# Optimization experiments

Hardware: AMD Instinct MI355X
Metric: run time of the kernel (lower is better)

The kernel has to match this reference:

```python
import jax, jax.numpy as jnp
import numpy as np

N, NF, D, H, L, FFN, E, EF = 2048, 64, 256, 8, 6, 1024, 32768, 16
HD = D // H
MAXDEG, MAXDIST = 64, 8


def setup_inputs() -> dict:
    key = jax.random.key(0)
    ks = jax.random.split(key, 32)
    s = 0.02
    nrm = lambda k, sh: (jax.random.normal(k, sh, jnp.float32) * s)
    return {
        "x": jax.random.normal(ks[0], (N, NF), jnp.float32),
        "edge_attr": jax.random.normal(ks[1], (E, EF), jnp.float32),
        "node_proj_w": nrm(ks[2], (D, NF)),
        "node_proj_b": jnp.zeros((D,), jnp.float32),
        "in_deg_emb": nrm(ks[3], (MAXDEG + 1, D)),
        "out_deg_emb": nrm(ks[4], (MAXDEG + 1, D)),
        "dist_bias": nrm(ks[5], (MAXDIST + 2, H)),
        "edge_proj_w": nrm(ks[6], (H, EF)),
        "edge_proj_b": jnp.zeros((H,), jnp.float32),
        "cls_token": nrm(ks[7], (1, D)),
        "q_w": nrm(ks[8], (L, D, D)), "q_b": jnp.zeros((L, D)),
        "k_w": nrm(ks[9], (L, D, D)), "k_b": jnp.zeros((L, D)),
        "v_w": nrm(ks[10], (L, D, D)), "v_b": jnp.zeros((L, D)),
        "o_w": nrm(ks[11], (L, D, D)), "o_b": jnp.zeros((L, D)),
        "ffn1_w": nrm(ks[12], (L, FFN, D)), "ffn1_b": jnp.zeros((L, FFN)),
        "ffn2_w": nrm(ks[13], (L, D, FFN)), "ffn2_b": jnp.zeros((L, D)),
        "ln1_s": jnp.ones((L, D)), "ln1_b": jnp.zeros((L, D)),
        "ln2_s": jnp.ones((L, D)), "ln2_b": jnp.zeros((L, D)),
        "fn_s": jnp.ones((D,)), "fn_b": jnp.zeros((D,)),
        "edge_index": jax.random.randint(ks[14], (2, E), 0, N, dtype=jnp.int32),
        "dist_matrix": jax.random.randint(ks[15], (N, N), 0, MAXDIST + 2, dtype=jnp.int32),
    }


def _ln(v, s, b):
    m = v.mean(-1, keepdims=True)
    va = v.var(-1, keepdims=True)
    return (v - m) / jnp.sqrt(va + 1e-5) * s + b


def _forward(x, edge_attr, node_proj_w, node_proj_b, in_deg_emb, out_deg_emb,
             dist_bias, edge_proj_w, edge_proj_b, cls_token,
             q_w, q_b, k_w, k_b, v_w, v_b, o_w, o_b,
             ffn1_w, ffn1_b, ffn2_w, ffn2_b,
             ln1_s, ln1_b, ln2_s, ln2_b, fn_s, fn_b,
             edge_index, dist_matrix):
    # node embedding + degree encoding
    h = x @ node_proj_w.T + node_proj_b  # (N, D)
    ones = jnp.ones((E,), jnp.int32)
    in_deg = jnp.clip(jax.ops.segment_sum(ones, edge_index[1], num_segments=N), 0, MAXDEG)
    out_deg = jnp.clip(jax.ops.segment_sum(ones, edge_index[0], num_segments=N), 0, MAXDEG)
    h = h + in_deg_emb[in_deg] + out_deg_emb[out_deg]
    h = jnp.concatenate([cls_token, h], axis=0)  # (N+1, D), CLS at row 0
    Nf = N + 1
    # spatial bias: pad dist matrix with zeros for CLS, then embed
    dist_p = jnp.pad(jnp.clip(dist_matrix, 0, MAXDIST + 1), ((1, 0), (1, 0)))
    bias = dist_bias[dist_p]  # (Nf, Nf, H)
    # edge-feature bias: scatter-add projected edge features into dense (N,N,H)
    proj = edge_attr @ edge_proj_w.T + edge_proj_b  # (E, H)
    ebias = jnp.zeros((N, N, H), h.dtype).at[edge_index[0], edge_index[1]].add(proj)
    bias = bias + jnp.pad(ebias, ((1, 0), (1, 0), (0, 0)))
    bias_t = bias.transpose(2, 0, 1)  # (H, Nf, Nf)
    scale = np.sqrt(HD).astype(np.float32)
    for l in range(L):
        hn = _ln(h, ln1_s[l], ln1_b[l])
        Q = (hn @ q_w[l].T + q_b[l]).reshape(Nf, H, HD).transpose(1, 0, 2)
        K = (hn @ k_w[l].T + k_b[l]).reshape(Nf, H, HD).transpose(1, 0, 2)
        V = (hn @ v_w[l].T + v_b[l]).reshape(Nf, H, HD).transpose(1, 0, 2)
        logits = jnp.einsum('hnd,hmd->hnm', Q, K) / scale + bias_t
        attn = jax.nn.softmax(logits, axis=-1)
        o = jnp.einsum('hnm,hmd->hnd', attn, V).transpose(1, 0, 2).reshape(Nf, D)
        h = h + o @ o_w[l].T + o_b[l]
        hn2 = _ln(h, ln2_s[l], ln2_b[l])
        h = h + jax.nn.gelu(hn2 @ ffn1_w[l].T + ffn1_b[l], approximate=False) @ ffn2_w[l].T + ffn2_b[l]
    h = _ln(h, fn_s, fn_b)
    return h, h[0]


def reference(x, edge_attr, node_proj_w, node_proj_b, in_deg_emb, out_deg_emb,
              dist_bias, edge_proj_w, edge_proj_b, cls_token,
              q_w, q_b, k_w, k_b, v_w, v_b, o_w, o_b,
              ffn1_w, ffn1_b, ffn2_w, ffn2_b,
              ln1_s, ln1_b, ln2_s, ln2_b, fn_s, fn_b,
              edge_index, dist_matrix):
    return _forward(x, edge_attr, node_proj_w, node_proj_b, in_deg_emb, out_deg_emb,
                    dist_bias, edge_proj_w, edge_proj_b, cls_token,
                    q_w, q_b, k_w, k_b, v_w, v_b, o_w, o_b,
                    ffn1_w, ffn1_b, ffn2_w, ffn2_b,
                    ln1_s, ln1_b, ln2_s, ln2_b, fn_s, fn_b,
                    edge_index, dist_matrix)
```

## Files before the change

kernel.cpp:

```cpp
#include <hip/hip_runtime.h>
#include <math.h>

#define N_ 2048
#define NF_IN 64
#define D_ 256
#define H_ 8
#define HD_ 32
#define L_ 6
#define FFN_ 1024
#define E_ 32768
#define EF_ 16
#define NF 2049
#define MAXDEG_ 64
#define BSTRIDE 2112
#define RPAD 2112
#define NSPLIT 4

typedef __attribute__((ext_vector_type(8))) short bf16x8;
typedef __attribute__((ext_vector_type(4))) float f32x4;

__device__ inline unsigned short f2b(float f){
  union { float f; unsigned u; } v; v.f = f;
  unsigned r = (v.u + 0x7fffu + ((v.u >> 16) & 1u)) >> 16;
  return (unsigned short)r;
}

__device__ inline unsigned char f2fp8(float f){
  unsigned u = __float_as_uint(f);
  unsigned s = (u >> 24) & 0x80u;
  float a = fabsf(f);
  if (a >= 448.f) return (unsigned char)(s | 0x7Eu);
  if (a < 0.015625f){
    int k = (int)rintf(a * 512.f);
    return (unsigned char)(s | (unsigned)k);
  }
  int e; float m = frexpf(a, &e);
  int E = e - 1;
  int m3 = (int)rintf(m * 16.f) - 8;
  if (m3 == 8){ E++; m3 = 0; }
  if (E > 8){ E = 8; m3 = 6; }
  if (E == 8 && m3 > 6) m3 = 6;
  return (unsigned char)(s | (unsigned)((E + 7) << 3) | (unsigned)m3);
}
__device__ inline float fp82f(unsigned char b){
  return __builtin_amdgcn_cvt_f32_fp8((int)b, 0);
}

__device__ inline void atomic_add_fp8(unsigned char* p, float add){
  unsigned* wp = (unsigned*)((size_t)p & ~(size_t)3);
  int sh = (int)((size_t)p & 3) * 8;
  unsigned old = *wp, assumed;
  do {
    assumed = old;
    unsigned char cur = (unsigned char)((assumed >> sh) & 0xFFu);
    float f = fp82f(cur) + add;
    unsigned nw = (assumed & ~(0xFFu << sh)) | ((unsigned)f2fp8(f) << sh);
    old = atomicCAS(wp, assumed, nw);
  } while (old != assumed);
}

__device__ inline float wred_sum(float v){
  #pragma unroll
  for (int o = 32; o > 0; o >>= 1) v += __shfl_down(v, o, 64);
  return v;
}

__global__ void zero_int(int* p, int n){
  int i = blockIdx.x * blockDim.x + threadIdx.x;
  if (i < n) p[i] = 0;
}

__global__ void deg_count(const int* __restrict__ ei, int* __restrict__ ind,
                          int* __restrict__ outd){
  int e = blockIdx.x * blockDim.x + threadIdx.x;
  if (e >= E_) return;
  atomicAdd(&outd[ei[e]], 1);
  atomicAdd(&ind[ei[E_ + e]], 1);
}

__global__ void embed_k(const float* __restrict__ x, const float* __restrict__ W,
                        const float* __restrict__ b, const float* __restrict__ inE,
                        const float* __restrict__ outE, const int* __restrict__ ind,
                        const int* __restrict__ outd, const float* __restrict__ cls,
                        float* __restrict__ h){
  int i = blockIdx.x, d = threadIdx.x;
  if (i == 0){ h[d] = cls[d]; return; }
  int n = i - 1;
  const float4* xr = (const float4*)(x + (long)n * NF_IN);
  const float4* wr = (const float4*)(W + (long)d * NF_IN);
  float acc = b[d];
  #pragma unroll
  for (int k = 0; k < NF_IN / 4; k++){
    float4 a = xr[k], w = wr[k];
    acc += a.x * w.x + a.y * w.y + a.z * w.z + a.w * w.w;
  }
  int id = min(ind[n], MAXDEG_), od = min(outd[n], MAXDEG_);
  acc += inE[(long)id * D_ + d] + outE[(long)od * D_ + d];
  h[(long)i * D_ + d] = acc;
}

__global__ void bias_fill(const int* __restrict__ dist, const float* __restrict__ db,
                          unsigned char* __restrict__ bb){
  __shared__ unsigned char lut8[10][H_];
  int i = blockIdx.x;
  if (threadIdx.x < 80) ((unsigned char*)lut8)[threadIdx.x] = f2fp8(db[threadIdx.x]);
  __syncthreads();
  for (int u = threadIdx.x; u < BSTRIDE / 8; u += 256){
    int dp[8];
    #pragma unroll
    for (int k = 0; k < 8; k++){
      int j = u * 8 + k;
      int d = 0;
      if (i > 0 && j > 0 && j < NF){
        int dv = dist[(long)(i - 1) * N_ + (j - 1)];
        d = max(0, min(dv, 9));
      }
      dp[k] = (j < NF) ? d : -1;
    }
    #pragma unroll
    for (int h = 0; h < H_; h++){
      unsigned lo = 0, hi = 0;
      #pragma unroll
      for (int k = 0; k < 4; k++){
        unsigned b0 = (dp[k] >= 0) ? lut8[dp[k]][h] : 0u;
        unsigned b1 = (dp[4 + k] >= 0) ? lut8[dp[4 + k]][h] : 0u;
        lo |= b0 << (8 * k);
        hi |= b1 << (8 * k);
      }
      *(uint2*)(bb + ((long)h * NF + i) * BSTRIDE + u * 8) = make_uint2(lo, hi);
    }
  }
}

__global__ void edge_bias(const float* __restrict__ ea, const float* __restrict__ W,
                          const float* __restrict__ b, const int* __restrict__ ei,
                          unsigned char* __restrict__ bb){
  int e = blockIdx.x * blockDim.x + threadIdx.x;
  if (e >= E_) return;
  float a[EF_];
  #pragma unroll
  for (int k = 0; k < EF_; k++) a[k] = ea[(long)e * EF_ + k];
  int src = ei[e], dst = ei[E_ + e];
  #pragma unroll
  for (int h = 0; h < H_; h++){
    float p = b[h];
    #pragma unroll
    for (int k = 0; k < EF_; k++) p += a[k] * W[h * EF_ + k];
    atomic_add_fp8(bb + ((long)h * NF + src + 1) * BSTRIDE + (dst + 1), p);
  }
}

__global__ void w2b_all(const float* __restrict__ qw, const float* __restrict__ kw,
                        const float* __restrict__ vw, const float* __restrict__ ow,
                        const float* __restrict__ f1w, const float* __restrict__ f2w,
                        short* __restrict__ wqkv, short* __restrict__ owb,
                        short* __restrict__ f1wb, short* __restrict__ f2wb){
  long i = (long)blockIdx.x * 256 + threadIdx.x;
  const long DD = (long)D_ * D_, LDD = (long)L_ * DD, LFD = (long)L_ * FFN_ * D_;
  if (i < LDD){
    long l = i / DD, r = i - l * DD;
    wqkv[l * 3 * DD + r]          = (short)f2b(qw[i]);
    wqkv[l * 3 * DD + DD + r]     = (short)f2b(kw[i]);
    wqkv[l * 3 * DD + 2 * DD + r] = (short)f2b(vw[i]);
    owb[i] = (short)f2b(ow[i]);
  }
  if (i < LFD){
    f1wb[i] = (short)f2b(f1w[i]);
    f2wb[i] = (short)f2b(f2w[i]);
  }
}

__global__ void ln_k(const float* __restrict__ in, const float* __restrict__ s,
                     const float* __restrict__ b, float* __restrict__ outf,
                     short* __restrict__ outb, int dup0){
  __shared__ float r1[4], r2[4];
  int i = blockIdx.x, d = threadIdx.x;
  float v = in[(long)i * D_ + d];
  float s1 = wred_sum(v), s2 = wred_sum(v * v);
  if ((d & 63) == 0){ r1[d >> 6] = s1; r2[d >> 6] = s2; }
  __syncthreads();
  float S1 = r1[0] + r1[1] + r1[2] + r1[3];
  float S2 = r2[0] + r2[1] + r2[2] + r2[3];
  float m = S1 * (1.0f / D_);
  float var = S2 * (1.0f / D_) - m * m;
  float y = (v - m) * rsqrtf(var + 1e-5f) * s[d] + b[d];
  if (outf){
    outf[(long)i * D_ + d] = y;
    if (dup0 && i == 0) outf[(long)NF * D_ + d] = y;
  }
  if (outb) outb[(long)i * D_ + d] = (short)f2b(y);
}

__global__ __launch_bounds__(256) void qkv_gemm(const short* __restrict__ A,
    const short* __restrict__ Wall, const float* __restrict__ qb,
    const float* __restrict__ kb, const float* __restrict__ vb,
    short* __restrict__ QKb, short* __restrict__ Vtg, int l){
  const int z = blockIdx.z;
  const short* W = Wall + ((long)(l * 3 + z)) * D_ * D_;
  const float* bsp = (z == 0) ? qb : (z == 1) ? kb : vb;
  __shared__ __align__(16) short As[64][40], Ws[64][40];
  const int tid = threadIdx.x, lane = tid & 63, wave = tid >> 6;
  const int col = lane & 15, quad = lane >> 4;
  const int wm = wave & 1, wn = wave >> 1;
  const int bm = blockIdx.x * 64, bn = blockIdx.y * 64;
  const f32x4 zero4 = {0.f, 0.f, 0.f, 0.f};
  f32x4 acc[2][2] = {{zero4, zero4}, {zero4, zero4}};
  const int row = tid >> 2, seg = tid & 3;
  for (int k0 = 0; k0 < D_; k0 += 32){
    __syncthreads();
    bf16x8 av = (bf16x8)(short)0;
    int gm = bm + row;
    if (gm < NF) av = *(const bf16x8*)(A + (long)gm * D_ + k0 + seg * 8);
    *(bf16x8*)&As[row][seg * 8] = av;
    *(bf16x8*)&Ws[row][seg * 8] = *(const bf16x8*)(W + (long)(bn + row) * D_ + k0 + seg * 8);
    __syncthreads();
    bf16x8 a0 = *(const bf16x8*)&As[wm * 32 + col][quad * 8];
    bf16x8 a1 = *(const bf16x8*)&As[wm * 32 + 16 + col][quad * 8];
    bf16x8 b0 = *(const bf16x8*)&Ws[wn * 32 + col][quad * 8];
    bf16x8 b1 = *(const bf16x8*)&Ws[wn * 32 + 16 + col][quad * 8];
    acc[0][0] = __builtin_amdgcn_mfma_f32_16x16x32_bf16(a0, b0, acc[0][0], 0, 0, 0);
    acc[0][1] = __builtin_amdgcn_mfma_f32_16x16x32_bf16(a0, b1, acc[0][1], 0, 0, 0);
    acc[1][0] = __builtin_amdgcn_mfma_f32_16x16x32_bf16(a1, b0, acc[1][0], 0, 0, 0);
    acc[1][1] = __builtin_amdgcn_mfma_f32_16x16x32_bf16(a1, b1, acc[1][1], 0, 0, 0);
  }
  #pragma unroll
  for (int i = 0; i < 2; i++)
    #pragma unroll
    for (int j = 0; j < 2; j++)
      #pragma unroll
      for (int r = 0; r < 4; r++){
        int gm = bm + wm * 32 + i * 16 + quad * 4 + r;
        if (gm >= NF) continue;
        int gn = bn + wn * 32 + j * 16 + col;
        float v = acc[i][j][r] + bsp[gn];
        if (z < 2) QKb[(long)z * NF * D_ + (long)gm * D_ + gn] = (short)f2b(v);
        else       Vtg[(long)gn * BSTRIDE + gm] = (short)f2b(v);
      }
}

template<int ACT, int ATOM, int MERGE>
__global__ __launch_bounds__(256) void mgemm(const short* __restrict__ A,
    const float* __restrict__ Op, const float* __restrict__ Lp,
    const short* __restrict__ W, const float* __restrict__ bs,
    float* __restrict__ Cf, short* __restrict__ Cb,
    int M, int Nn, int Kc, int Kstride){
  __shared__ __align__(16) short As[64][40], Ws[64][40];
  const int tid = threadIdx.x, lane = tid & 63, wave = tid >> 6;
  const int col = lane & 15, quad = lane >> 4;
  const int wm = wave & 1, wn = wave >> 1;
  const int bm = blockIdx.x * 64, bn = blockIdx.y * 64;
  const int koff = blockIdx.z * Kc;
  const f32x4 zero4 = {0.f, 0.f, 0.f, 0.f};
  f32x4 acc[2][2] = {{zero4, zero4}, {zero4, zero4}};
  const int row = tid >> 2, seg = tid & 3;
  for (int k0 = 0; k0 < Kc; k0 += 32){
    __syncthreads();
    int gm = bm + row;
    if (MERGE){
      int kg = koff + k0 + seg * 8;
      int hh = kg >> 5, d0 = kg & 31;
      short sarr[8] = {0,0,0,0,0,0,0,0};
      if (gm < M){
        float o0=0,o1=0,o2=0,o3=0,o4=0,o5=0,o6=0,o7=0, sl=0.f;
        #pragma unroll
        for (int q = 0; q < NSPLIT; q++){
          long rb = (long)(q * H_ + hh) * RPAD + gm;
          const float* op = Op + rb * HD_ + d0;
          float4 v0 = *(const float4*)op, v1 = *(const float4*)(op + 4);
          o0 += v0.x; o1 += v0.y; o2 += v0.z; o3 += v0.w;
          o4 += v1.x; o5 += v1.y; o6 += v1.z; o7 += v1.w;
          sl += Lp[rb];
        }
        float inv = 1.0f / sl;
        sarr[0]=(short)f2b(o0*inv); sarr[1]=(short)f2b(o1*inv);
        sarr[2]=(short)f2b(o2*inv); sarr[3]=(short)f2b(o3*inv);
        sarr[4]=(short)f2b(o4*inv); sarr[5]=(short)f2b(o5*inv);
        sarr[6]=(short)f2b(o6*inv); sarr[7]=(short)f2b(o7*inv);
      }
      *(bf16x8*)&As[row][seg * 8] = *(bf16x8*)sarr;
    } else {
      bf16x8 av = (bf16x8)(short)0;
      if (gm < M) av = *(const bf16x8*)(A + (long)gm * Kstride + koff + k0 + seg * 8);
      *(bf16x8*)&As[row][seg * 8] = av;
    }
    *(bf16x8*)&Ws[row][seg * 8] =
      *(const bf16x8*)(W + (long)(bn + row) * Kstride + koff + k0 + seg * 8);
    __syncthreads();
    bf16x8 a0 = *(const bf16x8*)&As[wm * 32 + col][quad * 8];
    bf16x8 a1 = *(const bf16x8*)&As[wm * 32 + 16 + col][quad * 8];
    bf16x8 b0 = *(const bf16x8*)&Ws[wn * 32 + col][quad * 8];
    bf16x8 b1 = *(const bf16x8*)&Ws[wn * 32 + 16 + col][quad * 8];
    acc[0][0] = __builtin_amdgcn_mfma_f32_16x16x32_bf16(a0, b0, acc[0][0], 0, 0, 0);
    acc[0][1] = __builtin_amdgcn_mfma_f32_16x16x32_bf16(a0, b1, acc[0][1], 0, 0, 0);
    acc[1][0] = __builtin_amdgcn_mfma_f32_16x16x32_bf16(a1, b0, acc[1][0], 0, 0, 0);
    acc[1][1] = __builtin_amdgcn_mfma_f32_16x16x32_bf16(a1, b1, acc[1][1], 0, 0, 0);
  }
  #pragma unroll
  for (int i = 0; i < 2; i++)
    #pragma unroll
    for (int j = 0; j < 2; j++)
      #pragma unroll
      for (int r = 0; r < 4; r++){
        int gm = bm + wm * 32 + i * 16 + quad * 4 + r;
        if (gm >= M) continue;
        int gn = bn + wn * 32 + j * 16 + col;
        if (ATOM){
          float v = acc[i][j][r] + (blockIdx.z == 0 ? bs[gn] : 0.f);
          atomicAdd(&Cf[(long)gm * Nn + gn], v);
        } else {
          float v = acc[i][j][r] + bs[gn];
          if (ACT == 1) v = v * 0.5f * (1.0f + erff(v * 0.70710678118654752f));
          Cb[(long)gm * Nn + gn] = (short)f2b(v);
        }
      }
}

__global__ __launch_bounds__(256) void fattn_k(const short* __restrict__ Qb,
    const short* __restrict__ Kb, const short* __restrict__ Vtg,
    const unsigned char* __restrict__ bias8, float* __restrict__ Opart,
    float* __restrict__ Lpart){
  __shared__ __align__(16) short Ks[64][40];
  __shared__ __align__(16) short Vt[32][72];
  __shared__ __align__(16) unsigned char PS[4][2304];

  const int tid = threadIdx.x, wave = tid >> 6, lane = tid & 63;
  const int col = lane & 15, quad = lane >> 4;
  const int h = blockIdx.y, qz = blockIdx.z;
  const int i0 = blockIdx.x * 64 + wave * 16;
  const int t0 = (qz == 0) ? 0 : 9 + 8 * (qz - 1);
  const int t1 = t0 + ((qz == 0) ? 9 : 8);

  int qrow = min(i0 + col, NF - 1);
  bf16x8 qf = *(const bf16x8*)(Qb + (long)qrow * D_ + h * HD_ + quad * 8);

  f32x4 oacc0 = {0.f, 0.f, 0.f, 0.f}, oacc1 = {0.f, 0.f, 0.f, 0.f};
  float rs[4] = {0.f, 0.f, 0.f, 0.f};
  const f32x4 zero4 = {0.f, 0.f, 0.f, 0.f};
  const float scale = 0.17677669529663687f;
  short* Pp = (short*)PS[wave];

  for (int t = t0; t < t1; t++){
    const int j0 = t * 64;
    __syncthreads();
    {
      int key = tid >> 2, seg = tid & 3;
      int j = j0 + key;
      bf16x8 kv = (bf16x8)(short)0;
      if (j < NF) kv = *(const bf16x8*)(Kb + (long)j * D_ + h * HD_ + seg * 8);
      *(bf16x8*)&Ks[key][seg * 8] = kv;
    }
    {
      int d = tid >> 3, seg = tid & 7;
      *(bf16x8*)&Vt[d][seg * 8] =
        *(const bf16x8*)(Vtg + (long)(h * HD_ + d) * BSTRIDE + j0 + seg * 8);
    }
    {
      int rw = lane >> 2, seg = lane & 3;
      int irow = min(i0 + rw, NF - 1);
      uint4 bv = *(const uint4*)(bias8 + (long)(h * NF + irow) * BSTRIDE + j0 + seg * 16);
      uint2* d2 = (uint2*)&PS[wave][rw * 80 + seg * 16];
      d2[0] = make_uint2(bv.x, bv.y);
      d2[1] = make_uint2(bv.z, bv.w);
    }
    __syncthreads();

    f32x4 sacc[4];
    #pragma unroll
    for (int t4 = 0; t4 < 4; t4++){
      bf16x8 kf = *(const bf16x8*)&Ks[t4 * 16 + col][quad * 8];
      sacc[t4] = __builtin_amdgcn_mfma_f32_16x16x32_bf16(qf, kf, zero4, 0, 0, 0);
    }

    const bool tail = (j0 + 64 > NF);
    #pragma unroll
    for (int r = 0; r < 4; r++){
      #pragma unroll
      for (int t4 = 0; t4 < 4; t4++){
        float bv = fp82f(PS[wave][(quad * 4 + r) * 80 + t4 * 16 + col]);
        float p = __expf(sacc[t4][r] * scale + bv);
        if (tail && (j0 + t4 * 16 + col >= NF)) p = 0.f;
        rs[r] += p;
        sacc[t4][r] = p;
      }
    }
    #pragma unroll
    for (int r = 0; r < 4; r++)
      #pragma unroll
      for (int t4 = 0; t4 < 4; t4++)
        Pp[(quad * 4 + r) * 72 + t4 * 16 + col] = (short)f2b(sacc[t4][r]);

    #pragma unroll
    for (int ks = 0; ks < 2; ks++){
      bf16x8 af = *(const bf16x8*)&Pp[col * 72 + ks * 32 + quad * 8];
      bf16x8 v0 = *(const bf16x8*)&Vt[col][ks * 32 + quad * 8];
      bf16x8 v1 = *(const bf16x8*)&Vt[16 + col][ks * 32 + quad * 8];
      oacc0 = __builtin_amdgcn_mfma_f32_16x16x32_bf16(af, v0, oacc0, 0, 0, 0);
      oacc1 = __builtin_amdgcn_mfma_f32_16x16x32_bf16(af, v1, oacc1, 0, 0, 0);
    }
  }

  #pragma unroll
  for (int r = 0; r < 4; r++){
    #pragma unroll
    for (int o = 1; o < 16; o <<= 1) rs[r] += __shfl_xor(rs[r], o, 64);
  }
  long pi = ((long)qz * H_ + h) * RPAD + i0 + quad * 4;
  #pragma unroll
  for (int r = 0; r < 4; r++){
    Opart[(pi + r) * HD_ + col] = oacc0[r];
    Opart[(pi + r) * HD_ + 16 + col] = oacc1[r];
    if (col == 0) Lpart[pi + r] = rs[r];
  }
}

extern "C" void kernel_launch(void* const* d_in, const int* in_sizes, int n_in,
                              void* d_out, int out_size, void* d_ws, size_t ws_size,
                              hipStream_t stream){
  const float* x    = (const float*)d_in[0];
  const float* ea   = (const float*)d_in[1];
  const float* npw  = (const float*)d_in[2];
  const float* npb  = (const float*)d_in[3];
  const float* inE  = (const float*)d_in[4];
  const float* outE = (const float*)d_in[5];
  const float* db   = (const float*)d_in[6];
  const float* epw  = (const float*)d_in[7];
  const float* epb  = (const float*)d_in[8];
  const float* cls  = (const float*)d_in[9];
  const float* qw   = (const float*)d_in[10];
  const float* qb   = (const float*)d_in[11];
  const float* kw   = (const float*)d_in[12];
  const float* kb   = (const float*)d_in[13];
  const float* vw   = (const float*)d_in[14];
  const float* vb   = (const float*)d_in[15];
  const float* ow   = (const float*)d_in[16];
  const float* ob   = (const float*)d_in[17];
  const float* f1w  = (const float*)d_in[18];
  const float* f1b  = (const float*)d_in[19];
  const float* f2w  = (const float*)d_in[20];
  const float* f2bp = (const float*)d_in[21];
  const float* ln1s = (const float*)d_in[22];
  const float* ln1b = (const float*)d_in[23];
  const float* ln2s = (const float*)d_in[24];
  const float* ln2b = (const float*)d_in[25];
  const float* fns  = (const float*)d_in[26];
  const float* fnb  = (const float*)d_in[27];
  const int*   ei   = (const int*)d_in[28];
  const int*   dist = (const int*)d_in[29];

  float* ws = (float*)d_ws;
  long off = 0;
  float* h     = ws + off; off += (long)NF * D_;
  float* Opart = ws + off; off += (long)NSPLIT * H_ * RPAD * HD_;
  float* Lpart = ws + off; off += (long)NSPLIT * H_ * RPAD;
  unsigned char* bias8 = (unsigned char*)(ws + off);
  off += ((long)H_ * NF * BSTRIDE + 3) / 4;
  short* hnb   = (short*)(ws + off); off += ((long)NF * D_ + 1) / 2;
  short* QKb   = (short*)(ws + off); off += (long)NF * D_;
  short* Vtg   = (short*)(ws + off); off += ((long)D_ * BSTRIDE + 1) / 2;
  short* midb  = (short*)(ws + off); off += ((long)NF * FFN_ + 1) / 2;
  short* wqkv  = (short*)(ws + off); off += ((long)3 * L_ * D_ * D_ + 1) / 2;
  short* owb   = (short*)(ws + off); off += ((long)L_ * D_ * D_ + 1) / 2;
  short* f1wb  = (short*)(ws + off); off += ((long)L_ * FFN_ * D_ + 1) / 2;
  short* f2wb  = (short*)(ws + off); off += ((long)L_ * FFN_ * D_ + 1) / 2;
  int*   ind   = (int*)(ws + off);
  int*   outd  = ind + N_;

  zero_int<<<(2 * N_ + 255) / 256, 256, 0, stream>>>(ind, 2 * N_);
  deg_count<<<(E_ + 255) / 256, 256, 0, stream>>>(ei, ind, outd);
  embed_k<<<NF, D_, 0, stream>>>(x, npw, npb, inE, outE, ind, outd, cls, h);
  bias_fill<<<NF, 256, 0, stream>>>(dist, db, bias8);
  edge_bias<<<(E_ + 255) / 256, 256, 0, stream>>>(ea, epw, epb, ei, bias8);
  {
    long LFD = (long)L_ * FFN_ * D_;
    w2b_all<<<(int)((LFD + 255) / 256), 256, 0, stream>>>(qw, kw, vw, ow, f1w, f2w,
                                                          wqkv, owb, f1wb, f2wb);
  }

  dim3 gQKV((NF + 63) / 64, D_ / 64, 3);
  dim3 gO((NF + 63) / 64, D_ / 64, 2);
  dim3 gF((NF + 63) / 64, FFN_ / 64, 1);
  dim3 gF2((NF + 63) / 64, D_ / 64, 4);
  dim3 gA((NF + 63) / 64, H_, NSPLIT);
  for (int l = 0; l < L_; l++){
    ln_k<<<NF, D_, 0, stream>>>(h, ln1s + l * D_, ln1b + l * D_, nullptr, hnb, 0);
    qkv_gemm<<<gQKV, 256, 0, stream>>>(hnb, wqkv, qb + l * D_, kb + l * D_, vb + l * D_,
                                       QKb, Vtg, l);
    fattn_k<<<gA, 256, 0, stream>>>(QKb, QKb + (long)NF * D_, Vtg, bias8, Opart, Lpart);
    mgemm<0,1,1><<<gO, 256, 0, stream>>>(nullptr, Opart, Lpart,
                                         owb + (long)l * D_ * D_, ob + l * D_,
                                         h, nullptr, NF, D_, 128, D_);
    ln_k<<<NF, D_, 0, stream>>>(h, ln2s + l * D_, ln2b + l * D_, nullptr, hnb, 0);
    mgemm<1,0,0><<<gF, 256, 0, stream>>>(hnb, nullptr, nullptr,
                                         f1wb + (long)l * FFN_ * D_, f1b + l * FFN_,
                                         nullptr, midb, NF, FFN_, D_, D_);
    mgemm<0,1,0><<<gF2, 256, 0, stream>>>(midb, nullptr, nullptr,
                                          f2wb + (long)l * FFN_ * D_, f2bp + l * D_,
                                          h, nullptr, NF, D_, 256, FFN_);
  }
  ln_k<<<NF, D_, 0, stream>>>(h, fns, fnb, (float*)d_out, nullptr, 1);
}
```

Baseline: 686.1 us.

## Fold softmax scale into Q and log2e into bias, load fp8 bias directly

Pre-multiplies Q by scale*log2e in the QKV epilogue and the distance/edge biases by log2e, so the attention kernel can use exp2f without a per-element multiply. The fp8 bias is now read straight from global memory into registers with hardware fp8-to-float conversion instead of being staged through LDS. Key columns are permuted so each lane owns four consecutive columns, which allows packed 8-byte P stores, and P is truncated rather than rounded to bf16 so the row sum matches the stored values. The risks are the changed rounding of Q and the fp8 bias after prescaling, plus LDS bank behaviour from the new padding.

```diff
diff --git a/kernel.cpp b/kernel.cpp
--- a/kernel.cpp
+++ b/kernel.cpp
@@ -15,6 +15,7 @@
 #define BSTRIDE 2112
 #define RPAD 2112
 #define NSPLIT 4
+#define LOG2E 1.4426950408889634f
 
 typedef __attribute__((ext_vector_type(8))) short bf16x8;
 typedef __attribute__((ext_vector_type(4))) float f32x4;
@@ -23,6 +24,10 @@
   union { float f; unsigned u; } v; v.f = f;
   unsigned r = (v.u + 0x7fffu + ((v.u >> 16) & 1u)) >> 16;
   return (unsigned short)r;
+}
+__device__ inline float b2f(short s){
+  union { unsigned u; float f; } v; v.u = ((unsigned)(unsigned short)s) << 16;
+  return v.f;
 }
 
 __device__ inline unsigned char f2fp8(float f){
@@ -103,7 +108,8 @@
                           unsigned char* __restrict__ bb){
   __shared__ unsigned char lut8[10][H_];
   int i = blockIdx.x;
-  if (threadIdx.x < 80) ((unsigned char*)lut8)[threadIdx.x] = f2fp8(db[threadIdx.x]);
+  if (threadIdx.x < 80)
+    ((unsigned char*)lut8)[threadIdx.x] = f2fp8(db[threadIdx.x] * LOG2E);
   __syncthreads();
   for (int u = threadIdx.x; u < BSTRIDE / 8; u += 256){
     int dp[8];
@@ -146,7 +152,7 @@
     float p = b[h];
     #pragma unroll
     for (int k = 0; k < EF_; k++) p += a[k] * W[h * EF_ + k];
-    atomic_add_fp8(bb + ((long)h * NF + src + 1) * BSTRIDE + (dst + 1), p);
+    atomic_add_fp8(bb + ((long)h * NF + src + 1) * BSTRIDE + (dst + 1), p * LOG2E);
   }
 }
 
@@ -223,6 +229,7 @@
     acc[1][0] = __builtin_amdgcn_mfma_f32_16x16x32_bf16(a1, b0, acc[1][0], 0, 0, 0);
     acc[1][1] = __builtin_amdgcn_mfma_f32_16x16x32_bf16(a1, b1, acc[1][1], 0, 0, 0);
   }
+  const float qscale = 0.25501133194822025f;
   #pragma unroll
   for (int i = 0; i < 2; i++)
     #pragma unroll
@@ -233,6 +240,7 @@
         if (gm >= NF) continue;
         int gn = bn + wn * 32 + j * 16 + col;
         float v = acc[i][j][r] + bsp[gn];
+        if (z == 0) v *= qscale;
         if (z < 2) QKb[(long)z * NF * D_ + (long)gm * D_ + gn] = (short)f2b(v);
         else       Vtg[(long)gn * BSTRIDE + gm] = (short)f2b(v);
       }
@@ -319,9 +327,9 @@
     const short* __restrict__ Kb, const short* __restrict__ Vtg,
     const unsigned char* __restrict__ bias8, float* __restrict__ Opart,
     float* __restrict__ Lpart){
-  __shared__ __align__(16) short Ks[64][40];
+  __shared__ __align__(16) short Ks[64][42];
   __shared__ __align__(16) short Vt[32][72];
-  __shared__ __align__(16) unsigned char PS[4][2304];
+  __shared__ __align__(16) short Ps[4][16][72];
 
   const int tid = threadIdx.x, wave = tid >> 6, lane = tid & 63;
   const int col = lane & 15, quad = lane >> 4;
@@ -333,14 +341,21 @@
   int qrow = min(i0 + col, NF - 1);
   bf16x8 qf = *(const bf16x8*)(Qb + (long)qrow * D_ + h * HD_ + quad * 8);
 
+  int brow[4];
+  #pragma unroll
+  for (int r = 0; r < 4; r++) brow[r] = min(i0 + quad * 4 + r, NF - 1);
+
   f32x4 oacc0 = {0.f, 0.f, 0.f, 0.f}, oacc1 = {0.f, 0.f, 0.f, 0.f};
   float rs[4] = {0.f, 0.f, 0.f, 0.f};
   const f32x4 zero4 = {0.f, 0.f, 0.f, 0.f};
-  const float scale = 0.17677669529663687f;
-  short* Pp = (short*)PS[wave];
+  short* Pp = &Ps[wave][0][0];
 
   for (int t = t0; t < t1; t++){
     const int j0 = t * 64;
+    unsigned bw[4];
+    #pragma unroll
+    for (int r = 0; r < 4; r++)
+      bw[r] = *(const unsigned*)(bias8 + (long)(h * NF + brow[r]) * BSTRIDE + j0 + col * 4);
     __syncthreads();
     {
       int key = tid >> 2, seg = tid & 3;
@@ -354,40 +369,36 @@
       *(bf16x8*)&Vt[d][seg * 8] =
         *(const bf16x8*)(Vtg + (long)(h * HD_ + d) * BSTRIDE + j0 + seg * 8);
     }
-    {
-      int rw = lane >> 2, seg = lane & 3;
-      int irow = min(i0 + rw, NF - 1);
-      uint4 bv = *(const uint4*)(bias8 + (long)(h * NF + irow) * BSTRIDE + j0 + seg * 16);
-      uint2* d2 = (uint2*)&PS[wave][rw * 80 + seg * 16];
-      d2[0] = make_uint2(bv.x, bv.y);
-      d2[1] = make_uint2(bv.z, bv.w);
-    }
     __syncthreads();
 
     f32x4 sacc[4];
     #pragma unroll
     for (int t4 = 0; t4 < 4; t4++){
-      bf16x8 kf = *(const bf16x8*)&Ks[t4 * 16 + col][quad * 8];
+      bf16x8 kf = *(const bf16x8*)&Ks[col * 4 + t4][quad * 8];
       sacc[t4] = __builtin_amdgcn_mfma_f32_16x16x32_bf16(qf, kf, zero4, 0, 0, 0);
     }
 
     const bool tail = (j0 + 64 > NF);
     #pragma unroll
     for (int r = 0; r < 4; r++){
+      float bv0 = __builtin_amdgcn_cvt_f32_fp8((int)bw[r], 0);
+      float bv1 = __builtin_amdgcn_cvt_f32_fp8((int)bw[r], 1);
+      float bv2 = __builtin_amdgcn_cvt_f32_fp8((int)bw[r], 2);
+      float bv3 = __builtin_amdgcn_cvt_f32_fp8((int)bw[r], 3);
+      float bvv[4] = {bv0, bv1, bv2, bv3};
+      unsigned short pb[4];
       #pragma unroll
       for (int t4 = 0; t4 < 4; t4++){
-        float bv = fp82f(PS[wave][(quad * 4 + r) * 80 + t4 * 16 + col]);
-        float p = __expf(sacc[t4][r] * scale + bv);
-        if (tail && (j0 + t4 * 16 + col >= NF)) p = 0.f;
-        rs[r] += p;
-        sacc[t4][r] = p;
+        float p = exp2f(sacc[t4][r] + bvv[t4]);
+        if (tail && (j0 + col * 4 + t4 >= NF)) p = 0.f;
+        unsigned pu = __float_as_uint(p) & 0xffff0000u;
+        rs[r] += __uint_as_float(pu);
+        pb[t4] = (unsigned short)(pu >> 16);
       }
-    }
-    #pragma unroll
-    for (int r = 0; r < 4; r++)
-      #pragma unroll
-      for (int t4 = 0; t4 < 4; t4++)
-        Pp[(quad * 4 + r) * 72 + t4 * 16 + col] = (short)f2b(sacc[t4][r]);
+      unsigned u0 = (unsigned)pb[0] | ((unsigned)pb[1] << 16);
+      unsigned u1 = (unsigned)pb[2] | ((unsigned)pb[3] << 16);
+      *(uint2*)&Pp[(quad * 4 + r) * 72 + col * 4] = make_uint2(u0, u1);
+    }
 
     #pragma unroll
     for (int ks = 0; ks < 2; ks++){
```

Measured after the change: 692.3 us. About the same (+0.9%).
